# Kernel optimization log

Measured on AMD Instinct MI355X. Metric: run time of the kernel, lower is better.

The kernel has to match this reference:

```python
import jax, jax.numpy as jnp
import numpy as np
import math

N_FILT = 80
FILT_DIM = 251
FS = 16000
MIN_FREQ = 50.0
MIN_BAND = 50.0


def _init_params():
    low_freq_mel = 80.0
    high_freq_mel = 2595.0 * np.log10(1.0 + FS / 2.0 / 700.0)
    mel_points = np.linspace(low_freq_mel, high_freq_mel, N_FILT)
    f_cos = 700.0 * (10.0 ** (mel_points / 2595.0) - 1.0)
    b1 = np.roll(f_cos, 1)
    b2 = np.roll(f_cos, -1)
    b1[0] = 30.0
    b2[-1] = FS / 2.0 - 100.0
    freq_scale = FS * 1.0
    return (jnp.asarray(b1 / freq_scale, dtype=jnp.float32),
            jnp.asarray((b2 - b1) / freq_scale, dtype=jnp.float32))


def setup_inputs() -> dict:
    key = jax.random.key(0)
    x = jax.random.normal(key, (32, 1, 32000), dtype=jnp.float32)
    filt_b1, filt_band = _init_params()
    return {"x": x, "filt_b1": filt_b1, "filt_band": filt_band}


def _sinc_batch(band, t_right):
    # band: [F] (in Hz, already scaled by fs); t_right: [T] (seconds)
    arg = 2.0 * math.pi * band[:, None] * t_right[None, :]  # [F, T]
    y_right = jnp.sin(arg) / arg
    y_left = y_right[:, ::-1]
    ones = jnp.ones((band.shape[0], 1), dtype=band.dtype)
    return jnp.concatenate([y_left, ones, y_right], axis=1)  # [F, 2T+1]


def _build_filters(filt_b1, filt_band):
    N = FILT_DIM
    freq_scale = float(FS)
    t_right = (jnp.linspace(1.0, (N - 1) / 2.0, (N - 1) // 2) / FS).astype(jnp.float32)
    filt_beg = jnp.abs(filt_b1) + MIN_FREQ / freq_scale            # [F]
    filt_end = filt_beg + (jnp.abs(filt_band) + MIN_BAND / freq_scale)
    # torch.linspace(0, N, steps=N): N points from 0 to N inclusive
    n = jnp.linspace(0.0, float(N), N).astype(jnp.float32)
    window = (0.54 - 0.46 * jnp.cos(2.0 * math.pi * n / N)).astype(jnp.float32)
    low_pass1 = 2.0 * filt_beg[:, None] * _sinc_batch(filt_beg * freq_scale, t_right)
    low_pass2 = 2.0 * filt_end[:, None] * _sinc_batch(filt_end * freq_scale, t_right)
    band_pass = low_pass2 - low_pass1                              # [F, N]
    band_pass = band_pass / jnp.max(band_pass, axis=1, keepdims=True)
    return band_pass * window[None, :]                             # [F, N]


def reference(x, filt_b1, filt_band):
    filters = _build_filters(filt_b1, filt_band)                   # [N_filt, Filt_dim]
    out = jax.lax.conv_general_dilated(
        x, filters[:, None, :],
        window_strides=(1,), padding='VALID',
        dimension_numbers=('NCH', 'OIH', 'NCH'))
    return out  # [B, N_filt, L - Filt_dim + 1]
```

## Files before the change

### kernel.cpp

```cpp
#include <hip/hip_runtime.h>
#include <math.h>

#define N_FILT   80
#define FILT_DIM 251
#define KPAD     256
#define SIG_LEN  32000
#define OUT_LEN  31750
#define BATCH    32
#define TPB      320

#define STRIP    1024
#define NREP     8
#define LROW     644
#define OBS2     36

#define TWO_PI_F 6.28318530717958647692f

typedef __attribute__((ext_vector_type(8))) short    short8;
typedef __attribute__((ext_vector_type(8))) _Float16 half8;
typedef __attribute__((ext_vector_type(4))) float    float4v;
typedef __attribute__((ext_vector_type(2))) float    float2v;

__global__ __launch_bounds__(256) void build_filters_kernel(
    const float* __restrict__ b1, const float* __restrict__ band,
    unsigned short* __restrict__ fh)
{
    const int f = blockIdx.x;
    const int i = threadIdx.x;

    const float MINF = 50.0f / 16000.0f;
    const float fb = fabsf(b1[f]) + MINF;
    const float fe = fb + fabsf(band[f]) + MINF;

    float v = 0.0f;
    if (i < FILT_DIM) {
        int m = i - 125; m = (m < 0) ? -m : m;
        if (m == 0) v = 2.0f * fe - 2.0f * fb;
        else {
            float a1 = TWO_PI_F * fb * (float)m;
            float a2 = TWO_PI_F * fe * (float)m;
            v = 2.0f * fe * (sinf(a2) / a2) - 2.0f * fb * (sinf(a1) / a1);
        }
    }

    __shared__ float red[256];
    red[i] = (i < FILT_DIM) ? v : -INFINITY;
    __syncthreads();
    #pragma unroll
    for (int s = 128; s > 0; s >>= 1) {
        if (i < s) red[i] = fmaxf(red[i], red[i + s]);
        __syncthreads();
    }
    const float mx = red[0];

    const float w   = 0.54f - 0.46f * cosf(TWO_PI_F * (float)i / 250.0f);
    const float val = (i < FILT_DIM) ? (v / mx) * w : 0.0f;
    const _Float16 h = (_Float16)val;
    fh[f * KPAD + i] = __builtin_bit_cast(unsigned short, h);
}

__global__ __launch_bounds__(TPB, 5) void sinc_mfma_kernel(
    const float* __restrict__ x,
    const unsigned short* __restrict__ fh,
    float* __restrict__ out)
{
    __shared__ __align__(16) unsigned xf[NREP * LROW];
    __shared__ __align__(16) float    ob[5][16 * OBS2];

    const int tid = threadIdx.x;
    const unsigned raw = blockIdx.x;
    const unsigned swz = (raw & 7u) * 128u + (raw >> 3);
    const int strip = (int)(swz & 31u);
    const int n     = (int)(swz >> 5);
    const int e0    = strip * STRIP;
    const float* xp = x + (size_t)n * SIG_LEN;

    for (int d = tid; d < LROW; d += TPB) {
        const int g = e0 + 2 * d;
        float v0, v1, v2;
        if (g + 2 < SIG_LEN) {
            float2 p = *(const float2*)(xp + g);
            v0 = p.x; v1 = p.y; v2 = xp[g + 2];
        } else {
            v0 = (g     < SIG_LEN) ? xp[g]     : 0.0f;
            v1 = (g + 1 < SIG_LEN) ? xp[g + 1] : 0.0f;
            v2 = (g + 2 < SIG_LEN) ? xp[g + 2] : 0.0f;
        }
        const _Float16 h0 = (_Float16)v0, h1 = (_Float16)v1, h2 = (_Float16)v2;
        union { _Float16 h[2]; unsigned u; } pe, po;
        pe.h[0] = h0; pe.h[1] = h1;
        po.h[0] = h1; po.h[1] = h2;
        xf[0 * LROW + d] = pe.u;
        xf[1 * LROW + d] = po.u;
        if (d >= 1) { xf[2 * LROW + d - 1] = pe.u;
                      xf[3 * LROW + d - 1] = po.u; }
        if (d >= 2) { xf[4 * LROW + d - 2] = pe.u;
                      xf[5 * LROW + d - 2] = po.u; }
        if (d >= 3) { xf[6 * LROW + d - 3] = pe.u;
                      xf[7 * LROW + d - 3] = po.u; }
    }

    const int lane = tid & 63;
    const int w    = tid >> 6;
    const int m    = lane & 15;
    const int q    = lane >> 4;
    short8 Ah[8];
    {
        const unsigned short* ph = fh + (w * 16 + m) * KPAD + q * 8;
        #pragma unroll
        for (int kb = 0; kb < 8; ++kb)
            Ah[kb] = *(const short8*)(ph + kb * 32);
    }
    __syncthreads();

    const int r = m & 7;
    const unsigned base = (unsigned)(r * LROW + 4 * (m >> 3) + 4 * q);

    float* const obw  = &ob[w][0];
    const int    cp   = 2 * (lane & 15);
    const int    rr0  = lane >> 4;
    const size_t row0 = ((size_t)n * N_FILT + w * 16) * OUT_LEN;

    for (int gp = 0; gp < 32; ++gp) {
        #pragma unroll
        for (int tl = 0; tl < 2; ++tl) {
            const int tt = gp * 2 + tl;
            float4v a0 = {0.f,0.f,0.f,0.f}, a1 = {0.f,0.f,0.f,0.f};
            const unsigned o0 = base + 8u * (unsigned)tt;
            #pragma unroll
            for (int kk = 0; kk < 4; ++kk) {
                a0 = __builtin_amdgcn_mfma_f32_16x16x32_f16(
                         __builtin_bit_cast(half8, Ah[2*kk]),
                         __builtin_bit_cast(half8, *(const uint4*)(&xf[o0 + 32*kk])),
                         a0, 0, 0, 0);
                a1 = __builtin_amdgcn_mfma_f32_16x16x32_f16(
                         __builtin_bit_cast(half8, Ah[2*kk+1]),
                         __builtin_bit_cast(half8, *(const uint4*)(&xf[o0 + 32*kk + 16])),
                         a1, 0, 0, 0);
            }
            const int oc = tl * 16 + m;
            #pragma unroll
            for (int rg = 0; rg < 4; ++rg)
                obw[(q * 4 + rg) * OBS2 + oc] = a0[rg] + a1[rg];
        }

        const int t0 = e0 + gp * 32 + cp;
        if (t0 + 1 < OUT_LEN) {
            #pragma unroll
            for (int j = 0; j < 4; ++j) {
                const int row = j * 4 + rr0;
                const float2v v = *(const float2v*)(&obw[row * OBS2 + cp]);
                *(float2v*)(out + row0 + (size_t)row * OUT_LEN + t0) = v;
            }
        }
    }
}

extern "C" void kernel_launch(void* const* d_in, const int* in_sizes, int n_in,
                              void* d_out, int out_size, void* d_ws, size_t ws_size,
                              hipStream_t stream)
{
    const float* x    = (const float*)d_in[0];
    const float* b1   = (const float*)d_in[1];
    const float* band = (const float*)d_in[2];
    float* outp = (float*)d_out;

    unsigned short* fh = (unsigned short*)d_ws;

    build_filters_kernel<<<dim3(N_FILT), dim3(256), 0, stream>>>(b1, band, fh);

    dim3 grid(32 * 32);
    sinc_mfma_kernel<<<grid, dim3(TPB), 0, stream>>>(x, fh, outp);
}
```

Measured before the change: 85.36 us.

## Prebuild fp16 pair replicas in global memory and read B operands directly

A new pre-pass converts the input signal to fp16 and writes two global planes of packed pairs (even and odd alignment). A new MFMA kernel then loads its B operands straight from global memory with unaligned 16-byte loads instead of staging eight shifted replicas in LDS. Work is split into one 16-filter by 1024-sample tile per wave across 2560 blocks of 128 threads. This removes the per-block LDS fill and its barrier and allows higher occupancy, at the cost of an extra kernel launch and heavier global/L2 read traffic. The old kernel is kept as a fallback when the workspace is too small.

```diff
diff --git a/kernel.cpp b/kernel.cpp
--- a/kernel.cpp
+++ b/kernel.cpp
@@ -7,12 +7,16 @@
 #define SIG_LEN  32000
 #define OUT_LEN  31750
 #define BATCH    32
-#define TPB      320
 
 #define STRIP    1024
+#define OBS2     36
+
+#define XRN      16512
+#define XRPLANE  (BATCH * XRN)
+#define WS_NEED  (40960u + 2u * XRPLANE * 4u)
+
 #define NREP     8
 #define LROW     644
-#define OBS2     36
 
 #define TWO_PI_F 6.28318530717958647692f
 
@@ -20,6 +24,9 @@
 typedef __attribute__((ext_vector_type(8))) _Float16 half8;
 typedef __attribute__((ext_vector_type(4))) float    float4v;
 typedef __attribute__((ext_vector_type(2))) float    float2v;
+typedef __attribute__((ext_vector_type(4))) unsigned uint4v;
+
+typedef struct __attribute__((packed, aligned(4))) { uint4v v; } uload16;
 
 __global__ __launch_bounds__(256) void build_filters_kernel(
     const float* __restrict__ b1, const float* __restrict__ band,
@@ -59,7 +66,99 @@
     fh[f * KPAD + i] = __builtin_bit_cast(unsigned short, h);
 }
 
-__global__ __launch_bounds__(TPB, 5) void sinc_mfma_kernel(
+__global__ __launch_bounds__(256) void build_x_replicas_kernel(
+    const float* __restrict__ x, unsigned* __restrict__ xr)
+{
+    const int n = blockIdx.y;
+    const int d = blockIdx.x * 256 + threadIdx.x;
+    if (d >= XRN) return;
+    const float* xp = x + (size_t)n * SIG_LEN;
+    const int e = 2 * d;
+    const float v0 = (e     < SIG_LEN) ? xp[e]     : 0.0f;
+    const float v1 = (e + 1 < SIG_LEN) ? xp[e + 1] : 0.0f;
+    const float v2 = (e + 2 < SIG_LEN) ? xp[e + 2] : 0.0f;
+    const _Float16 h0 = (_Float16)v0, h1 = (_Float16)v1, h2 = (_Float16)v2;
+    union { _Float16 h[2]; unsigned u; } pe, po;
+    pe.h[0] = h0; pe.h[1] = h1;
+    po.h[0] = h1; po.h[1] = h2;
+    xr[0 * XRPLANE + n * XRN + d] = pe.u;
+    xr[1 * XRPLANE + n * XRN + d] = po.u;
+}
+
+__global__ __launch_bounds__(128, 8) void sinc_mfma_g_kernel(
+    const unsigned short* __restrict__ fh,
+    const unsigned* __restrict__ xr,
+    float* __restrict__ out)
+{
+    __shared__ __align__(16) float ob[2][16 * OBS2];
+
+    const int tid  = threadIdx.x;
+    const int wv   = tid >> 6;
+    const int lane = tid & 63;
+
+    const unsigned bswz = (blockIdx.x & 7u) * 320u + (blockIdx.x >> 3);
+    const unsigned i    = bswz * 2u + (unsigned)wv;
+    const int n     = (int)(i / 160u);
+    const int rem   = (int)(i % 160u);
+    const int fb    = rem >> 5;
+    const int strip = rem & 31;
+    const int e0    = strip * STRIP;
+
+    const int m = lane & 15;
+    const int q = lane >> 4;
+
+    short8 Ah[8];
+    {
+        const unsigned short* ph = fh + (fb * 16 + m) * KPAD + q * 8;
+        #pragma unroll
+        for (int kb = 0; kb < 8; ++kb)
+            Ah[kb] = *(const short8*)(ph + kb * 32);
+    }
+
+    const unsigned* bp = xr + (unsigned)(m & 1) * XRPLANE + (unsigned)n * XRN
+                            + (unsigned)(e0 >> 1) + (unsigned)(m >> 1) + 4u * q;
+
+    float* const obw  = &ob[wv][0];
+    const int    cp   = 2 * (lane & 15);
+    const int    rr0  = lane >> 4;
+    const size_t row0 = ((size_t)n * N_FILT + fb * 16) * OUT_LEN;
+
+    for (int gp = 0; gp < 32; ++gp) {
+        #pragma unroll
+        for (int tl = 0; tl < 2; ++tl) {
+            const int tt = gp * 2 + tl;
+            float4v a0 = {0.f,0.f,0.f,0.f}, a1 = {0.f,0.f,0.f,0.f};
+            const unsigned o0 = 8u * (unsigned)tt;
+            #pragma unroll
+            for (int kk = 0; kk < 4; ++kk) {
+                const uint4v b0 = ((const uload16*)(bp + o0 + 32u*kk))->v;
+                const uint4v b1 = ((const uload16*)(bp + o0 + 32u*kk + 16u))->v;
+                a0 = __builtin_amdgcn_mfma_f32_16x16x32_f16(
+                         __builtin_bit_cast(half8, Ah[2*kk]),
+                         __builtin_bit_cast(half8, b0), a0, 0, 0, 0);
+                a1 = __builtin_amdgcn_mfma_f32_16x16x32_f16(
+                         __builtin_bit_cast(half8, Ah[2*kk+1]),
+                         __builtin_bit_cast(half8, b1), a1, 0, 0, 0);
+            }
+            const int oc = tl * 16 + m;
+            #pragma unroll
+            for (int rg = 0; rg < 4; ++rg)
+                obw[(q * 4 + rg) * OBS2 + oc] = a0[rg] + a1[rg];
+        }
+
+        const int t0 = e0 + gp * 32 + cp;
+        if (t0 + 1 < OUT_LEN) {
+            #pragma unroll
+            for (int j = 0; j < 4; ++j) {
+                const int row = j * 4 + rr0;
+                const float2v v = *(const float2v*)(&obw[row * OBS2 + cp]);
+                *(float2v*)(out + row0 + (size_t)row * OUT_LEN + t0) = v;
+            }
+        }
+    }
+}
+
+__global__ __launch_bounds__(320, 5) void sinc_mfma_kernel(
     const float* __restrict__ x,
     const unsigned short* __restrict__ fh,
     float* __restrict__ out)
@@ -75,7 +174,7 @@
     const int e0    = strip * STRIP;
     const float* xp = x + (size_t)n * SIG_LEN;
 
-    for (int d = tid; d < LROW; d += TPB) {
+    for (int d = tid; d < LROW; d += 320) {
         const int g = e0 + 2 * d;
         float v0, v1, v2;
         if (g + 2 < SIG_LEN) {
@@ -166,9 +265,15 @@
     float* outp = (float*)d_out;
 
     unsigned short* fh = (unsigned short*)d_ws;
+    unsigned*       xr = (unsigned*)((char*)d_ws + 40960);
 
     build_filters_kernel<<<dim3(N_FILT), dim3(256), 0, stream>>>(b1, band, fh);
 
-    dim3 grid(32 * 32);
-    sinc_mfma_kernel<<<grid, dim3(TPB), 0, stream>>>(x, fh, outp);
-}
+    if (ws_size >= (size_t)WS_NEED) {
+        build_x_replicas_kernel<<<dim3((XRN + 255) / 256, BATCH), dim3(256),
+                                  0, stream>>>(x, xr);
+        sinc_mfma_g_kernel<<<dim3(2560), dim3(128), 0, stream>>>(fh, xr, outp);
+    } else {
+        sinc_mfma_kernel<<<dim3(1024), dim3(320), 0, stream>>>(x, fh, outp);
+    }
+}
```

Result: slower. 184.5 us (+116.2%).

## Realign output stores to cache-line boundaries and halve strip size

Applied to the files above, without the earlier changes.

Each output row begins at an address that is not a multiple of 32 floats. The store phase now shifts each row's write window by a row-dependent offset so the global float2 stores fall on 128-byte-aligned segments. To support this, a two-half staging buffer carries results across consecutive 32-column groups, and there are explicit prologue and epilogue stores. The strip length is halved to 512 and the grid doubled to 2048 blocks, which gives more parallelism at the cost of reloading the input halo more often.

```diff
diff --git a/kernel.cpp b/kernel.cpp
--- a/kernel.cpp
+++ b/kernel.cpp
@@ -9,10 +9,11 @@
 #define BATCH    32
 #define TPB      320
 
-#define STRIP    1024
+#define STRIP    512
+#define NGRP     16
 #define NREP     8
-#define LROW     644
-#define OBS2     36
+#define LROW     388
+#define OBS3     68
 
 #define TWO_PI_F 6.28318530717958647692f
 
@@ -65,13 +66,13 @@
     float* __restrict__ out)
 {
     __shared__ __align__(16) unsigned xf[NREP * LROW];
-    __shared__ __align__(16) float    ob[5][16 * OBS2];
+    __shared__ __align__(16) float    ob[5][16 * OBS3];
 
     const int tid = threadIdx.x;
     const unsigned raw = blockIdx.x;
-    const unsigned swz = (raw & 7u) * 128u + (raw >> 3);
-    const int strip = (int)(swz & 31u);
-    const int n     = (int)(swz >> 5);
+    const unsigned swz = (raw & 7u) * 256u + (raw >> 3);
+    const int strip = (int)(swz & 63u);
+    const int n     = (int)(swz >> 6);
     const int e0    = strip * STRIP;
     const float* xp = x + (size_t)n * SIG_LEN;
 
@@ -121,39 +122,85 @@
     const int    rr0  = lane >> 4;
     const size_t row0 = ((size_t)n * N_FILT + w * 16) * OUT_LEN;
 
-    for (int gp = 0; gp < 32; ++gp) {
+    float* prow[1]; (void)prow;
+
+    #define COMPUTE_GROUP(gv)                                                  \
+    {                                                                          \
+        const int hbase_ = ((gv) & 1) * 34;                                    \
+        _Pragma("unroll")                                                      \
+        for (int tl = 0; tl < 2; ++tl) {                                       \
+            const int tt = (gv) * 2 + tl;                                      \
+            float4v a0 = {0.f,0.f,0.f,0.f}, a1 = {0.f,0.f,0.f,0.f};            \
+            const unsigned o0 = base + 8u * (unsigned)tt;                      \
+            _Pragma("unroll")                                                  \
+            for (int kk = 0; kk < 4; ++kk) {                                   \
+                a0 = __builtin_amdgcn_mfma_f32_16x16x32_f16(                   \
+                         __builtin_bit_cast(half8, Ah[2*kk]),                  \
+                         __builtin_bit_cast(half8,                             \
+                             *(const uint4*)(&xf[o0 + 32*kk])),                \
+                         a0, 0, 0, 0);                                         \
+                a1 = __builtin_amdgcn_mfma_f32_16x16x32_f16(                   \
+                         __builtin_bit_cast(half8, Ah[2*kk+1]),                \
+                         __builtin_bit_cast(half8,                             \
+                             *(const uint4*)(&xf[o0 + 32*kk + 16])),           \
+                         a1, 0, 0, 0);                                         \
+            }                                                                  \
+            const int oc = hbase_ + tl * 16 + m;                               \
+            _Pragma("unroll")                                                  \
+            for (int rg = 0; rg < 4; ++rg)                                     \
+                obw[(q * 4 + rg) * OBS3 + oc] = a0[rg] + a1[rg];               \
+        }                                                                      \
+    }
+
+    COMPUTE_GROUP(0);
+    #pragma unroll
+    for (int j = 0; j < 4; ++j) {
+        const int row   = 4 * j + rr0;
+        const int shift = (26 * row) & 31;
+        if (cp < shift) {
+            const int t = e0 + cp;
+            if (t + 1 < OUT_LEN) {
+                const float2v v = *(const float2v*)(&obw[row * OBS3 + cp]);
+                *(float2v*)(out + row0 + (size_t)row * OUT_LEN + t) = v;
+            }
+        }
+    }
+
+    #pragma unroll 2
+    for (int k = 0; k < 15; ++k) {
+        COMPUTE_GROUP(k + 1);
+        const int hcur  = (k & 1) * 34;
+        const int hnext = 34 - hcur;
         #pragma unroll
-        for (int tl = 0; tl < 2; ++tl) {
-            const int tt = gp * 2 + tl;
-            float4v a0 = {0.f,0.f,0.f,0.f}, a1 = {0.f,0.f,0.f,0.f};
-            const unsigned o0 = base + 8u * (unsigned)tt;
-            #pragma unroll
-            for (int kk = 0; kk < 4; ++kk) {
-                a0 = __builtin_amdgcn_mfma_f32_16x16x32_f16(
-                         __builtin_bit_cast(half8, Ah[2*kk]),
-                         __builtin_bit_cast(half8, *(const uint4*)(&xf[o0 + 32*kk])),
-                         a0, 0, 0, 0);
-                a1 = __builtin_amdgcn_mfma_f32_16x16x32_f16(
-                         __builtin_bit_cast(half8, Ah[2*kk+1]),
-                         __builtin_bit_cast(half8, *(const uint4*)(&xf[o0 + 32*kk + 16])),
-                         a1, 0, 0, 0);
+        for (int j = 0; j < 4; ++j) {
+            const int row   = 4 * j + rr0;
+            const int shift = (26 * row) & 31;
+            const int sc    = shift + cp;
+            const int hb    = (sc < 32) ? hcur : hnext;
+            const int col   = sc & 31;
+            const int t     = e0 + 32 * k + sc;
+            if (t + 1 < OUT_LEN) {
+                const float2v v =
+                    *(const float2v*)(&obw[row * OBS3 + hb + col]);
+                *(float2v*)(out + row0 + (size_t)row * OUT_LEN + t) = v;
             }
-            const int oc = tl * 16 + m;
-            #pragma unroll
-            for (int rg = 0; rg < 4; ++rg)
-                obw[(q * 4 + rg) * OBS2 + oc] = a0[rg] + a1[rg];
-        }
-
-        const int t0 = e0 + gp * 32 + cp;
-        if (t0 + 1 < OUT_LEN) {
-            #pragma unroll
-            for (int j = 0; j < 4; ++j) {
-                const int row = j * 4 + rr0;
-                const float2v v = *(const float2v*)(&obw[row * OBS2 + cp]);
-                *(float2v*)(out + row0 + (size_t)row * OUT_LEN + t0) = v;
+        }
+    }
+
+    #pragma unroll
+    for (int j = 0; j < 4; ++j) {
+        const int row   = 4 * j + rr0;
+        const int shift = (26 * row) & 31;
+        const int sc    = shift + cp;
+        if (sc < 32) {
+            const int t = e0 + 480 + sc;
+            if (t + 1 < OUT_LEN) {
+                const float2v v = *(const float2v*)(&obw[row * OBS3 + 34 + sc]);
+                *(float2v*)(out + row0 + (size_t)row * OUT_LEN + t) = v;
             }
         }
     }
+    #undef COMPUTE_GROUP
 }
 
 extern "C" void kernel_launch(void* const* d_in, const int* in_sizes, int n_in,
@@ -169,6 +216,6 @@
 
     build_filters_kernel<<<dim3(N_FILT), dim3(256), 0, stream>>>(b1, band, fh);
 
-    dim3 grid(32 * 32);
+    dim3 grid(2048);
     sinc_mfma_kernel<<<grid, dim3(TPB), 0, stream>>>(x, fh, outp);
 }
```

Measured after the change: 255.4 us. 199% more time.
